# Performance work log

Measured on AMD Instinct MI355X. Metric: run time of the kernel, lower is better.

The kernel has to match this reference:

```python
import jax, jax.numpy as jnp
import numpy as np

B, C, H, W = 32, 2048, 24, 24
P, RED = 4, 16


def setup_inputs() -> dict:
    key = jax.random.key(0)
    ks = jax.random.split(key, 7)
    return {
        "x": jax.random.normal(ks[0], (B, C, H, W), dtype=jnp.float32),
        "fc1_w": jax.random.normal(ks[1], (C // RED, C), dtype=jnp.float32) * 0.02,
        "fc1_b": jax.random.normal(ks[2], (C // RED,), dtype=jnp.float32) * 0.02,
        "fc2_w": jax.random.normal(ks[3], (C * P, C // RED), dtype=jnp.float32) * 0.02,
        "fc2_b": jax.random.normal(ks[4], (C * P,), dtype=jnp.float32) * 0.02,
        "conv_w": jax.random.normal(ks[5], (C,), dtype=jnp.float32) * 0.02,
        "conv_b": jax.random.normal(ks[6], (C,), dtype=jnp.float32) * 0.02,
    }


def reference(x, fc1_w, fc1_b, fc2_w, fc2_b, conv_w, conv_b):
    # SE-style dynamic weight generation
    pooled = x.mean(axis=(2, 3))                                  # (B, C)
    hidden = jax.nn.silu(pooled @ fc1_w.T + fc1_b)                # (B, C//red)
    dw = (hidden @ fc2_w.T + fc2_b).reshape(B, P, C)              # (B, P, C)
    # depthwise 1x1 conv == per-channel scale + bias
    base = x * conv_w[None, :, None, None] + conv_b[None, :, None, None]
    # per-part channel-weighted reduction: out[b,p,h,w] = sum_c base[b,c,h,w]*dw[b,p,c]
    out = jnp.einsum('bchw,bpc->bphw', base, dw)                  # (B, P, H, W)
    return jax.nn.softmax(out, axis=1)
```

## Files before the change

kernel.cpp:

```cpp
#include <hip/hip_runtime.h>
#include <hip/hip_bf16.h>
#include <math.h>

#define B_ 32
#define C_ 2048
#define HW_ 576
#define P_ 4
#define HID_ 128

__global__ void pool_kernel(const float* __restrict__ x, float* __restrict__ pooled) {
    int gwave = blockIdx.x * 4 + (threadIdx.x >> 6);
    int lane  = threadIdx.x & 63;
    const float4* xp4 = (const float4*)(x + (size_t)gwave * HW_);
    float s = 0.f;
    for (int i = lane; i < HW_ / 4; i += 64) {
        float4 v = xp4[i];
        s += v.x + v.y + v.z + v.w;
    }
    #pragma unroll
    for (int off = 32; off > 0; off >>= 1) s += __shfl_down(s, off, 64);
    if (lane == 0) pooled[gwave] = s * (1.0f / (float)HW_);
}

__global__ void fc1_kernel(const float* __restrict__ pooled, const float* __restrict__ w,
                           const float* __restrict__ bias, float* __restrict__ hidden) {
    int o    = blockIdx.x * 4 + (threadIdx.x >> 6);
    int lane = threadIdx.x & 63;
    int b = o >> 7;
    int j = o & 127;
    const float* pr = pooled + (size_t)b * C_;
    const float* wr = w + (size_t)j * C_;
    float s = 0.f;
    for (int k = lane; k < C_; k += 64) s += pr[k] * wr[k];
    #pragma unroll
    for (int off = 32; off > 0; off >>= 1) s += __shfl_down(s, off, 64);
    if (lane == 0) {
        float z = s + bias[j];
        hidden[o] = z / (1.0f + expf(-z));
    }
}

__global__ void fc2_kernel(const float* __restrict__ hidden, const float* __restrict__ w,
                           const float* __restrict__ bias, float* __restrict__ dw) {
    int o    = blockIdx.x * 4 + (threadIdx.x >> 6);
    int lane = threadIdx.x & 63;
    int b = o >> 13;
    int j = o & 8191;
    const float* hr = hidden + (size_t)b * HID_;
    const float* wr = w + (size_t)j * HID_;
    float s = hr[lane] * wr[lane] + hr[lane + 64] * wr[lane + 64];
    #pragma unroll
    for (int off = 32; off > 0; off >>= 1) s += __shfl_down(s, off, 64);
    if (lane == 0) dw[o] = s + bias[j];
}

__global__ void biasc_kernel(const float* __restrict__ conv_b, const float* __restrict__ dw,
                             float* __restrict__ bias_const) {
    int o    = blockIdx.x * 4 + (threadIdx.x >> 6);
    int lane = threadIdx.x & 63;
    const float* dr = dw + (size_t)o * C_;
    float s = 0.f;
    for (int k = lane; k < C_; k += 64) s += conv_b[k] * dr[k];
    #pragma unroll
    for (int off = 32; off > 0; off >>= 1) s += __shfl_down(s, off, 64);
    if (lane == 0) bias_const[o] = s;
}

__global__ void einsum_kernel(const float* __restrict__ x, const float* __restrict__ conv_w,
                              const float* __restrict__ dw, float* __restrict__ accum) {
    int b     = blockIdx.x;
    int chunk = blockIdx.y;
    int c0    = chunk * 64;
    int tid   = threadIdx.x;

    __shared__ float4 m4[64];
    if (tid < 64) {
        float cw = conv_w[c0 + tid];
        const float* dr = dw + (size_t)b * (P_ * C_) + c0 + tid;
        float4 v;
        v.x = cw * dr[0 * C_];
        v.y = cw * dr[1 * C_];
        v.z = cw * dr[2 * C_];
        v.w = cw * dr[3 * C_];
        m4[tid] = v;
    }
    __syncthreads();

    const float* xp = x + ((size_t)b * C_ + c0) * HW_ + tid;
    float a0 = 0.f, a1 = 0.f, a2 = 0.f, a3 = 0.f;
    #pragma unroll 8
    for (int c = 0; c < 64; ++c) {
        float v = xp[(size_t)c * HW_];
        float4 m = m4[c];
        a0 += v * m.x;
        a1 += v * m.y;
        a2 += v * m.z;
        a3 += v * m.w;
    }
    float* ap = accum + ((size_t)b * P_) * HW_ + tid;
    atomicAdd(ap + 0 * HW_, a0);
    atomicAdd(ap + 1 * HW_, a1);
    atomicAdd(ap + 2 * HW_, a2);
    atomicAdd(ap + 3 * HW_, a3);
}

__global__ void softmax_kernel(const float* __restrict__ accum, const float* __restrict__ bias_const,
                               float* __restrict__ out) {
    int idx = blockIdx.x * 256 + threadIdx.x;
    int b  = idx / HW_;
    int hw = idx - b * HW_;
    const float* ap = accum + ((size_t)b * P_) * HW_ + hw;
    const float* bc = bias_const + b * P_;
    float v0 = ap[0 * HW_] + bc[0];
    float v1 = ap[1 * HW_] + bc[1];
    float v2 = ap[2 * HW_] + bc[2];
    float v3 = ap[3 * HW_] + bc[3];
    float mx = fmaxf(fmaxf(v0, v1), fmaxf(v2, v3));
    float e0 = expf(v0 - mx), e1 = expf(v1 - mx), e2 = expf(v2 - mx), e3 = expf(v3 - mx);
    float inv = 1.0f / (e0 + e1 + e2 + e3);
    float* op = out + ((size_t)b * P_) * HW_ + hw;
    op[0 * HW_] = e0 * inv;
    op[1 * HW_] = e1 * inv;
    op[2 * HW_] = e2 * inv;
    op[3 * HW_] = e3 * inv;
}

extern "C" void kernel_launch(void* const* d_in, const int* in_sizes, int n_in,
                              void* d_out, int out_size, void* d_ws, size_t ws_size,
                              hipStream_t stream) {
    const float* x      = (const float*)d_in[0];
    const float* fc1_w  = (const float*)d_in[1];
    const float* fc1_b  = (const float*)d_in[2];
    const float* fc2_w  = (const float*)d_in[3];
    const float* fc2_b  = (const float*)d_in[4];
    const float* conv_w = (const float*)d_in[5];
    const float* conv_b = (const float*)d_in[6];
    float* out = (float*)d_out;

    float* ws      = (float*)d_ws;
    float* pooled  = ws;
    float* hidden  = pooled + 65536;
    float* dw      = hidden + 4096;
    float* bias_c  = dw + 262144;
    float* accum   = bias_c + 128;

    hipMemsetAsync(accum, 0, (size_t)B_ * P_ * HW_ * sizeof(float), stream);

    pool_kernel<<<16384, 256, 0, stream>>>(x, pooled);
    fc1_kernel<<<1024, 256, 0, stream>>>(pooled, fc1_w, fc1_b, hidden);
    fc2_kernel<<<65536, 256, 0, stream>>>(hidden, fc2_w, fc2_b, dw);
    biasc_kernel<<<32, 256, 0, stream>>>(conv_b, dw, bias_c);
    einsum_kernel<<<dim3(B_, 32), 576, 0, stream>>>(x, conv_w, dw, accum);
    softmax_kernel<<<72, 256, 0, stream>>>(accum, bias_c, out);
}
```

Before: 301.8 us.

## Replace einsum atomics with per-slot partials, vectorize x loads, restructure fc2 grid

The einsum kernel now covers 256 channels per block in four channel groups, each thread loading float4 pixels. It writes per-slot partial sums to a workspace instead of doing atomicAdd into a zeroed accumulator, and the softmax kernel sums the 32 slots before normalizing, which drops the memset. fc2 now uses 256 blocks that stage the hidden vector in shared memory and loop over 256 outputs per wave, instead of launching 65536 tiny blocks. The trade-offs are extra partial-buffer traffic and lower einsum and fc2 parallelism: 256 blocks each, with a serial 256-row loop per fc2 wave.

```diff
diff --git a/kernel.cpp b/kernel.cpp
--- a/kernel.cpp
+++ b/kernel.cpp
@@ -7,6 +7,8 @@
 #define HW_ 576
 #define P_ 4
 #define HID_ 128
+#define NCHUNK_ 8
+#define NSLOT_ 32
 
 __global__ void pool_kernel(const float* __restrict__ x, float* __restrict__ pooled) {
     int gwave = blockIdx.x * 4 + (threadIdx.x >> 6);
@@ -42,16 +44,25 @@
 
 __global__ void fc2_kernel(const float* __restrict__ hidden, const float* __restrict__ w,
                            const float* __restrict__ bias, float* __restrict__ dw) {
-    int o    = blockIdx.x * 4 + (threadIdx.x >> 6);
-    int lane = threadIdx.x & 63;
-    int b = o >> 13;
-    int j = o & 8191;
-    const float* hr = hidden + (size_t)b * HID_;
-    const float* wr = w + (size_t)j * HID_;
-    float s = hr[lane] * wr[lane] + hr[lane + 64] * wr[lane + 64];
-    #pragma unroll
-    for (int off = 32; off > 0; off >>= 1) s += __shfl_down(s, off, 64);
-    if (lane == 0) dw[o] = s + bias[j];
+    int b  = blockIdx.x >> 3;
+    int jc = blockIdx.x & 7;
+    int tid = threadIdx.x;
+    int wave = tid >> 6, lane = tid & 63;
+
+    __shared__ float h[HID_];
+    if (tid < HID_) h[tid] = hidden[(size_t)b * HID_ + tid];
+    __syncthreads();
+    float h0 = h[lane], h1 = h[lane + 64];
+
+    int jbase = jc * 1024 + wave * 256;
+    for (int i = 0; i < 256; ++i) {
+        int j = jbase + i;
+        const float* wr = w + (size_t)j * HID_;
+        float s = h0 * wr[lane] + h1 * wr[lane + 64];
+        #pragma unroll
+        for (int off = 32; off > 0; off >>= 1) s += __shfl_down(s, off, 64);
+        if (lane == 0) dw[(size_t)b * (P_ * C_) + j] = s + bias[j];
+    }
 }
 
 __global__ void biasc_kernel(const float* __restrict__ conv_b, const float* __restrict__ dw,
@@ -67,14 +78,14 @@
 }
 
 __global__ void einsum_kernel(const float* __restrict__ x, const float* __restrict__ conv_w,
-                              const float* __restrict__ dw, float* __restrict__ accum) {
+                              const float* __restrict__ dw, float* __restrict__ part) {
     int b     = blockIdx.x;
     int chunk = blockIdx.y;
-    int c0    = chunk * 64;
+    int c0    = chunk * 256;
     int tid   = threadIdx.x;
 
-    __shared__ float4 m4[64];
-    if (tid < 64) {
+    __shared__ float4 m4[256];
+    if (tid < 256) {
         float cw = conv_w[c0 + tid];
         const float* dr = dw + (size_t)b * (P_ * C_) + c0 + tid;
         float4 v;
@@ -86,35 +97,45 @@
     }
     __syncthreads();
 
-    const float* xp = x + ((size_t)b * C_ + c0) * HW_ + tid;
-    float a0 = 0.f, a1 = 0.f, a2 = 0.f, a3 = 0.f;
-    #pragma unroll 8
-    for (int c = 0; c < 64; ++c) {
-        float v = xp[(size_t)c * HW_];
+    int g = tid / 144;
+    int i = tid - g * 144;
+
+    float4 a0 = {0,0,0,0}, a1 = {0,0,0,0}, a2 = {0,0,0,0}, a3 = {0,0,0,0};
+    const float* xb = x + ((size_t)b * C_ + c0) * HW_;
+    #pragma unroll 4
+    for (int k = 0; k < 64; ++k) {
+        int c = g + 4 * k;
+        float4 v = ((const float4*)(xb + (size_t)c * HW_))[i];
         float4 m = m4[c];
-        a0 += v * m.x;
-        a1 += v * m.y;
-        a2 += v * m.z;
-        a3 += v * m.w;
+        a0.x += v.x * m.x; a0.y += v.y * m.x; a0.z += v.z * m.x; a0.w += v.w * m.x;
+        a1.x += v.x * m.y; a1.y += v.y * m.y; a1.z += v.z * m.y; a1.w += v.w * m.y;
+        a2.x += v.x * m.z; a2.y += v.y * m.z; a2.z += v.z * m.z; a2.w += v.w * m.z;
+        a3.x += v.x * m.w; a3.y += v.y * m.w; a3.z += v.z * m.w; a3.w += v.w * m.w;
     }
-    float* ap = accum + ((size_t)b * P_) * HW_ + tid;
-    atomicAdd(ap + 0 * HW_, a0);
-    atomicAdd(ap + 1 * HW_, a1);
-    atomicAdd(ap + 2 * HW_, a2);
-    atomicAdd(ap + 3 * HW_, a3);
+    int slot = chunk * 4 + g;
+    float4* pp = (float4*)(part + (((size_t)b * NSLOT_ + slot) * P_) * HW_) + i;
+    pp[0 * (HW_ / 4)] = a0;
+    pp[1 * (HW_ / 4)] = a1;
+    pp[2 * (HW_ / 4)] = a2;
+    pp[3 * (HW_ / 4)] = a3;
 }
 
-__global__ void softmax_kernel(const float* __restrict__ accum, const float* __restrict__ bias_const,
+__global__ void softmax_kernel(const float* __restrict__ part, const float* __restrict__ bias_const,
                                float* __restrict__ out) {
     int idx = blockIdx.x * 256 + threadIdx.x;
     int b  = idx / HW_;
     int hw = idx - b * HW_;
-    const float* ap = accum + ((size_t)b * P_) * HW_ + hw;
     const float* bc = bias_const + b * P_;
-    float v0 = ap[0 * HW_] + bc[0];
-    float v1 = ap[1 * HW_] + bc[1];
-    float v2 = ap[2 * HW_] + bc[2];
-    float v3 = ap[3 * HW_] + bc[3];
+    float v0 = bc[0], v1 = bc[1], v2 = bc[2], v3 = bc[3];
+    const float* pb = part + ((size_t)b * NSLOT_ * P_) * HW_ + hw;
+    #pragma unroll 8
+    for (int s = 0; s < NSLOT_; ++s) {
+        const float* ps = pb + (size_t)s * P_ * HW_;
+        v0 += ps[0 * HW_];
+        v1 += ps[1 * HW_];
+        v2 += ps[2 * HW_];
+        v3 += ps[3 * HW_];
+    }
     float mx = fmaxf(fmaxf(v0, v1), fmaxf(v2, v3));
     float e0 = expf(v0 - mx), e1 = expf(v1 - mx), e2 = expf(v2 - mx), e3 = expf(v3 - mx);
     float inv = 1.0f / (e0 + e1 + e2 + e3);
@@ -142,14 +163,12 @@
     float* hidden  = pooled + 65536;
     float* dw      = hidden + 4096;
     float* bias_c  = dw + 262144;
-    float* accum   = bias_c + 128;
-
-    hipMemsetAsync(accum, 0, (size_t)B_ * P_ * HW_ * sizeof(float), stream);
+    float* part    = bias_c + 128;
 
     pool_kernel<<<16384, 256, 0, stream>>>(x, pooled);
     fc1_kernel<<<1024, 256, 0, stream>>>(pooled, fc1_w, fc1_b, hidden);
-    fc2_kernel<<<65536, 256, 0, stream>>>(hidden, fc2_w, fc2_b, dw);
+    fc2_kernel<<<256, 256, 0, stream>>>(hidden, fc2_w, fc2_b, dw);
     biasc_kernel<<<32, 256, 0, stream>>>(conv_b, dw, bias_c);
-    einsum_kernel<<<dim3(B_, 32), 576, 0, stream>>>(x, conv_w, dw, accum);
-    softmax_kernel<<<72, 256, 0, stream>>>(accum, bias_c, out);
+    einsum_kernel<<<dim3(B_, NCHUNK_), 576, 0, stream>>>(x, conv_w, dw, part);
+    softmax_kernel<<<72, 256, 0, stream>>>(part, bias_c, out);
 }
```

New measurement: 476.2 us. 1.58x slower.
